# Kernel tuning notes

Hardware: AMD Instinct MI355X
Metric: run time of the kernel (lower is better)

## Reference

```python
import jax, jax.numpy as jnp
import numpy as np

WIDTH = [512, 512, 512, 512]
GRID_SIZE = 5
K = 3  # spline order
GRID_RANGE = (-1.0, 1.0)
BATCH = 1024


def extend_grid(grid, k):
    # grid: (I, G+1) -> (I, G+2k+1), extend k knots on each side with uniform step h
    h = (grid[:, -1:] - grid[:, :1]) / (grid.shape[1] - 1)
    for _ in range(k):
        grid = jnp.concatenate([grid[:, :1] - h, grid, grid[:, -1:] + h], axis=1)
    return grid


def b_spline_basis(x, grid, k):
    # Cox-de Boor recursion. x: (B, I), grid: (I, G+2k+1) -> (B, I, G+k)
    xe = x[:, :, None]
    g = grid[None, :, :]
    B = ((xe >= g[:, :, :-1]) & (xe < g[:, :, 1:])).astype(x.dtype)
    for p in range(1, k + 1):
        B = ((xe - g[:, :, :-(p + 1)]) / (g[:, :, p:-1] - g[:, :, :-(p + 1)]) * B[:, :, :-1]
             + (g[:, :, p + 1:] - xe) / (g[:, :, p + 1:] - g[:, :, 1:-p]) * B[:, :, 1:])
    return B


def kan_layer(x, grid, coef, sb, sp):
    # x: (B, I); coef: (I, O, G+k); sb, sp: (I, O)
    base = jax.nn.silu(x)                              # residual b(x), (B, I)
    Bmat = b_spline_basis(x, grid, K)                  # (B, I, G+k)
    y = jnp.einsum('bik,iok->bio', Bmat, coef)         # spline curves, (B, I, O)
    post = sb[None] * base[:, :, None] + sp[None] * y  # postacts (B, I, O)
    return post.sum(axis=1)                            # (B, O)


def setup_inputs() -> dict:
    key = jax.random.key(0)
    ks = jax.random.split(key, 1 + 2 * (len(WIDTH) - 1))
    inp = {"x": jax.random.normal(ks[0], (BATCH, WIDTH[0]), dtype=jnp.float32)}
    for l, (i, o) in enumerate(zip(WIDTH[:-1], WIDTH[1:])):
        base = jnp.linspace(GRID_RANGE[0], GRID_RANGE[1], GRID_SIZE + 1, dtype=jnp.float32)
        grid = extend_grid(jnp.broadcast_to(base[None], (i, GRID_SIZE + 1)), K)
        kc, kb = ks[1 + 2 * l], ks[2 + 2 * l]
        inp[f"grid{l}"] = grid
        inp[f"coef{l}"] = jax.random.normal(kc, (i, o, GRID_SIZE + K), dtype=jnp.float32) * (0.1 / GRID_SIZE)
        inp[f"sb{l}"] = (jax.random.uniform(kb, (i, o), dtype=jnp.float32) * 2.0 - 1.0) / np.sqrt(i).astype(np.float32)
        inp[f"sp{l}"] = jnp.ones((i, o), dtype=jnp.float32) / np.sqrt(i).astype(np.float32)
    return inp


def reference(x, grid0, coef0, sb0, sp0, grid1, coef1, sb1, sp1, grid2, coef2, sb2, sp2):
    x = kan_layer(x, grid0, coef0, sb0, sp0)
    x = kan_layer(x, grid1, coef1, sb1, sp1)
    x = kan_layer(x, grid2, coef2, sb2, sp2)
    return x
```

## Files before the change

### kernel.cpp

```cpp
#include <hip/hip_runtime.h>
#include <hip/hip_bf16.h>

#define I_DIM  512
#define O_DIM  512
#define NBATCH 1024
#define NSPL   8
#define KPI    12
#define KDIM   (I_DIM * KPI)
#define NGRID  12

typedef __attribute__((ext_vector_type(8))) short bf16x8;
typedef __attribute__((ext_vector_type(4))) float f32x4;

__device__ __forceinline__ void gload_lds16(const __hip_bfloat16* g, __hip_bfloat16* l) {
    __builtin_amdgcn_global_load_lds(
        (const __attribute__((address_space(1))) void*)g,
        (__attribute__((address_space(3))) void*)l, 16, 0, 0);
}

__global__ void build_wt_all(const float* __restrict__ c0, const float* __restrict__ b0, const float* __restrict__ p0,
                             const float* __restrict__ c1, const float* __restrict__ b1, const float* __restrict__ p1,
                             const float* __restrict__ c2, const float* __restrict__ b2, const float* __restrict__ p2,
                             __hip_bfloat16* __restrict__ Wt) {
    int l = blockIdx.y;
    const float* coef = l == 0 ? c0 : (l == 1 ? c1 : c2);
    const float* sb   = l == 0 ? b0 : (l == 1 ? b1 : b2);
    const float* sp   = l == 0 ? p0 : (l == 1 ? p1 : p2);
    __hip_bfloat16* W = Wt + (size_t)l * O_DIM * KDIM;

    int tid = blockIdx.x * blockDim.x + threadIdx.x;
    int i = tid & (I_DIM - 1);
    int o = tid >> 9;
    float sbv = sb[i * O_DIM + o];
    float spv = sp[i * O_DIM + o];
    const float* cf = coef + (size_t)(i * O_DIM + o) * NSPL;
    __align__(16) __hip_bfloat16 row[KPI];
#pragma unroll
    for (int k = 0; k < NSPL; ++k) row[k] = __float2bfloat16(spv * cf[k]);
    __hip_bfloat16 whi = __float2bfloat16(sbv);
    __hip_bfloat16 wlo = __float2bfloat16(sbv - __bfloat162float(whi));
    row[8]  = whi;
    row[9]  = wlo;
    row[10] = whi;
    row[11] = __float2bfloat16(0.0f);
    uint2* dst = (uint2*)(W + (size_t)o * KDIM + i * KPI);
    const uint2* src = (const uint2*)row;
    dst[0] = src[0]; dst[1] = src[1]; dst[2] = src[2];
}

#define SPLITK 8

__device__ __forceinline__ void features_core(float xv, const float* __restrict__ grid,
                                              int i, __hip_bfloat16* __restrict__ dst) {
    float g[NGRID];
#pragma unroll
    for (int j = 0; j < NGRID; ++j) g[j] = grid[i * NGRID + j];

    float B[NGRID - 1];
#pragma unroll
    for (int j = 0; j < NGRID - 1; ++j)
        B[j] = (xv >= g[j] && xv < g[j + 1]) ? 1.0f : 0.0f;
#pragma unroll
    for (int p = 1; p <= 3; ++p) {
#pragma unroll
        for (int j = 0; j < NGRID - 1 - p; ++j) {
            B[j] = (xv - g[j]) / (g[j + p] - g[j]) * B[j]
                 + (g[j + p + 1] - xv) / (g[j + p + 1] - g[j + 1]) * B[j + 1];
        }
    }
    float s = xv / (1.0f + __expf(-xv));
    __hip_bfloat16 shi = __float2bfloat16(s);
    __hip_bfloat16 slo = __float2bfloat16(s - __bfloat162float(shi));

    __align__(16) __hip_bfloat16 row[KPI];
#pragma unroll
    for (int k = 0; k < NSPL; ++k) row[k] = __float2bfloat16(B[k]);
    row[8]  = shi;
    row[9]  = shi;
    row[10] = slo;
    row[11] = __float2bfloat16(0.0f);

    uint2* d = (uint2*)dst;
    const uint2* srow = (const uint2*)row;
    d[0] = srow[0]; d[1] = srow[1]; d[2] = srow[2];
}

__global__ void build_features_x(const float* __restrict__ x,
                                 const float* __restrict__ grid,
                                 __hip_bfloat16* __restrict__ F) {
    int tid = blockIdx.x * blockDim.x + threadIdx.x;
    features_core(x[tid], grid, tid & (I_DIM - 1), F + (size_t)tid * KPI);
}

__global__ void build_features_sum(const float* __restrict__ P,
                                   const float* __restrict__ grid,
                                   __hip_bfloat16* __restrict__ F) {
    int tid = blockIdx.x * blockDim.x + threadIdx.x;
    float xv = 0.f;
#pragma unroll
    for (int s = 0; s < SPLITK; ++s) xv += P[(size_t)s * NBATCH * I_DIM + tid];
    features_core(xv, grid, tid & (I_DIM - 1), F + (size_t)tid * KPI);
}

__global__ void reduce_out(const float* __restrict__ P, float* __restrict__ out) {
    int tid = blockIdx.x * blockDim.x + threadIdx.x;
    float v = 0.f;
#pragma unroll
    for (int s = 0; s < SPLITK; ++s) v += P[(size_t)s * NBATCH * O_DIM + tid];
    out[tid] = v;
}

#define BM 128
#define BN 64
#define BK 64
#define KSEG (KDIM / SPLITK)

__global__ __launch_bounds__(256)
void gemm_kernel(const __hip_bfloat16* __restrict__ A,
                 const __hip_bfloat16* __restrict__ Wt,
                 float* __restrict__ P) {
    __shared__ __hip_bfloat16 lA[BM * BK];
    __shared__ __hip_bfloat16 lB[BN * BK];

    int bm = blockIdx.x;
    int bn = blockIdx.y;
    int ks = blockIdx.z;
    int tid = threadIdx.x;
    int lane = tid & 63;
    int wave = tid >> 6;
    int wr = (wave & 1) * 64;
    int wc = (wave >> 1) * 32;
    int q  = lane >> 4;
    int ln = lane & 15;

    f32x4 acc[4][2];
#pragma unroll
    for (int a = 0; a < 4; ++a)
#pragma unroll
        for (int b = 0; b < 2; ++b) acc[a][b] = (f32x4){0.f, 0.f, 0.f, 0.f};

    const __hip_bfloat16* Abase = A  + (size_t)(bm * BM) * KDIM + ks * KSEG;
    const __hip_bfloat16* Bbase = Wt + (size_t)(bn * BN) * KDIM + ks * KSEG;

    for (int kt = 0; kt < KSEG; kt += BK) {
        __syncthreads();
#pragma unroll
        for (int c = 0; c < 4; ++c) {
            int cc = wave * 256 + c * 64 + lane;
            int r = cc >> 3, j = (cc & 7) ^ (r & 7);
            gload_lds16(Abase + (size_t)r * KDIM + kt + j * 8,
                        lA + (size_t)(wave * 256 + c * 64) * 8);
        }
#pragma unroll
        for (int c = 0; c < 2; ++c) {
            int cc = wave * 128 + c * 64 + lane;
            int r = cc >> 3, j = (cc & 7) ^ (r & 7);
            gload_lds16(Bbase + (size_t)r * KDIM + kt + j * 8,
                        lB + (size_t)(wave * 128 + c * 64) * 8);
        }
        __syncthreads();

#pragma unroll
        for (int kh = 0; kh < 2; ++kh) {
            bf16x8 af[4], bfr[2];
#pragma unroll
            for (int rt = 0; rt < 4; ++rt) {
                int row = wr + rt * 16 + ln;
                af[rt] = *(const bf16x8*)(lA + row * BK + (((kh * 4 + q) ^ (row & 7)) * 8));
            }
#pragma unroll
            for (int ct = 0; ct < 2; ++ct) {
                int row = wc + ct * 16 + ln;
                bfr[ct] = *(const bf16x8*)(lB + row * BK + (((kh * 4 + q) ^ (row & 7)) * 8));
            }
#pragma unroll
            for (int rt = 0; rt < 4; ++rt)
#pragma unroll
                for (int ct = 0; ct < 2; ++ct)
                    acc[rt][ct] = __builtin_amdgcn_mfma_f32_16x16x32_bf16(
                        af[rt], bfr[ct], acc[rt][ct], 0, 0, 0);
        }
    }

    float* Pp = P + (size_t)ks * NBATCH * O_DIM;
    int orow = bm * BM + wr;
    int ocol = bn * BN + wc + ln;
#pragma unroll
    for (int rt = 0; rt < 4; ++rt)
#pragma unroll
        for (int ct = 0; ct < 2; ++ct)
#pragma unroll
            for (int r = 0; r < 4; ++r)
                Pp[(size_t)(orow + rt * 16 + q * 4 + r) * O_DIM + ocol + ct * 16]
                    = acc[rt][ct][r];
}

extern "C" void kernel_launch(void* const* d_in, const int* in_sizes, int n_in,
                              void* d_out, int out_size, void* d_ws, size_t ws_size,
                              hipStream_t stream) {
    const float* x0      = (const float*)d_in[0];
    const float* grid[3] = {(const float*)d_in[1], (const float*)d_in[5], (const float*)d_in[9]};
    const float* coef[3] = {(const float*)d_in[2], (const float*)d_in[6], (const float*)d_in[10]};
    const float* sb[3]   = {(const float*)d_in[3], (const float*)d_in[7], (const float*)d_in[11]};
    const float* sp[3]   = {(const float*)d_in[4], (const float*)d_in[8], (const float*)d_in[12]};

    char* ws = (char*)d_ws;
    const size_t wt_bytes = (size_t)O_DIM * KDIM * sizeof(__hip_bfloat16);
    const size_t f_bytes  = (size_t)NBATCH * KDIM * sizeof(__hip_bfloat16);
    __hip_bfloat16* Wt = (__hip_bfloat16*)ws;
    __hip_bfloat16* F  = (__hip_bfloat16*)(ws + 3 * wt_bytes);
    float* P = (float*)(ws + 3 * wt_bytes + f_bytes);

    build_wt_all<<<dim3((I_DIM * O_DIM) / 256, 3), 256, 0, stream>>>(
        coef[0], sb[0], sp[0], coef[1], sb[1], sp[1], coef[2], sb[2], sp[2], Wt);

    build_features_x<<<(NBATCH * I_DIM) / 256, 256, 0, stream>>>(x0, grid[0], F);
    gemm_kernel<<<dim3(NBATCH / BM, O_DIM / BN, SPLITK), 256, 0, stream>>>(F, Wt, P);

    for (int l = 1; l < 3; ++l) {
        build_features_sum<<<(NBATCH * I_DIM) / 256, 256, 0, stream>>>(P, grid[l], F);
        gemm_kernel<<<dim3(NBATCH / BM, O_DIM / BN, SPLITK), 256, 0, stream>>>(
            F, Wt + (size_t)l * O_DIM * KDIM, P);
    }
    reduce_out<<<(NBATCH * O_DIM) / 256, 256, 0, stream>>>(P, (float*)d_out);
}
```

Before: 202.3 us.

## Fuse all KAN layers into one cooperative persistent kernel with grid syncs

Replaces the sequence of eight separate launches (weight build, feature build, three split-K GEMMs, reductions) with a single cooperative kernel. It uses 256 blocks of 512 threads, and grid-wide barriers separate the phases. The GEMM tile is widened to 128x128 per block so the fixed grid covers every tile, and a fallback launch path is kept if the cooperative launch fails. This removes per-launch overhead and inter-kernel gaps. In exchange, each GEMM phase has fewer, larger blocks with one-block-per-CU occupancy, and grid syncs add their own cost.

Result: slower. 420.0 us (+107.6%).

```diff
diff --git a/kernel.cpp b/kernel.cpp
--- a/kernel.cpp
+++ b/kernel.cpp
@@ -1,5 +1,8 @@
 #include <hip/hip_runtime.h>
 #include <hip/hip_bf16.h>
+#include <hip/hip_cooperative_groups.h>
+
+namespace cg = cooperative_groups;
 
 #define I_DIM  512
 #define O_DIM  512
@@ -8,6 +11,13 @@
 #define KPI    12
 #define KDIM   (I_DIM * KPI)
 #define NGRID  12
+#define SPLITK 8
+#define KSEG   (KDIM / SPLITK)
+#define BK     64
+
+#define NBLK 256
+#define TPB  512
+#define NTH  (NBLK * TPB)
 
 typedef __attribute__((ext_vector_type(8))) short bf16x8;
 typedef __attribute__((ext_vector_type(4))) float f32x4;
@@ -18,19 +28,46 @@
         (__attribute__((address_space(3))) void*)l, 16, 0, 0);
 }
 
-__global__ void build_wt_all(const float* __restrict__ c0, const float* __restrict__ b0, const float* __restrict__ p0,
-                             const float* __restrict__ c1, const float* __restrict__ b1, const float* __restrict__ p1,
-                             const float* __restrict__ c2, const float* __restrict__ b2, const float* __restrict__ p2,
-                             __hip_bfloat16* __restrict__ Wt) {
-    int l = blockIdx.y;
-    const float* coef = l == 0 ? c0 : (l == 1 ? c1 : c2);
-    const float* sb   = l == 0 ? b0 : (l == 1 ? b1 : b2);
-    const float* sp   = l == 0 ? p0 : (l == 1 ? p1 : p2);
-    __hip_bfloat16* W = Wt + (size_t)l * O_DIM * KDIM;
-
-    int tid = blockIdx.x * blockDim.x + threadIdx.x;
-    int i = tid & (I_DIM - 1);
-    int o = tid >> 9;
+__device__ __forceinline__ void features_core(float xv, const float* __restrict__ grid,
+                                              int i, __hip_bfloat16* __restrict__ dst) {
+    float g[NGRID];
+#pragma unroll
+    for (int j = 0; j < NGRID; ++j) g[j] = grid[i * NGRID + j];
+
+    float B[NGRID - 1];
+#pragma unroll
+    for (int j = 0; j < NGRID - 1; ++j)
+        B[j] = (xv >= g[j] && xv < g[j + 1]) ? 1.0f : 0.0f;
+#pragma unroll
+    for (int p = 1; p <= 3; ++p) {
+#pragma unroll
+        for (int j = 0; j < NGRID - 1 - p; ++j) {
+            B[j] = (xv - g[j]) / (g[j + p] - g[j]) * B[j]
+                 + (g[j + p + 1] - xv) / (g[j + p + 1] - g[j + 1]) * B[j + 1];
+        }
+    }
+    float s = xv / (1.0f + __expf(-xv));
+    __hip_bfloat16 shi = __float2bfloat16(s);
+    __hip_bfloat16 slo = __float2bfloat16(s - __bfloat162float(shi));
+
+    __align__(16) __hip_bfloat16 row[KPI];
+#pragma unroll
+    for (int k = 0; k < NSPL; ++k) row[k] = __float2bfloat16(B[k]);
+    row[8]  = shi;
+    row[9]  = shi;
+    row[10] = slo;
+    row[11] = __float2bfloat16(0.0f);
+
+    uint2* d = (uint2*)dst;
+    const uint2* srow = (const uint2*)row;
+    d[0] = srow[0]; d[1] = srow[1]; d[2] = srow[2];
+}
+
+__device__ __forceinline__ void wt_row_core(const float* __restrict__ coef,
+                                            const float* __restrict__ sb,
+                                            const float* __restrict__ sp,
+                                            int i, int o,
+                                            __hip_bfloat16* __restrict__ W) {
     float sbv = sb[i * O_DIM + o];
     float spv = sp[i * O_DIM + o];
     const float* cf = coef + (size_t)(i * O_DIM + o) * NSPL;
@@ -48,41 +85,171 @@
     dst[0] = src[0]; dst[1] = src[1]; dst[2] = src[2];
 }
 
-#define SPLITK 8
-
-__device__ __forceinline__ void features_core(float xv, const float* __restrict__ grid,
-                                              int i, __hip_bfloat16* __restrict__ dst) {
-    float g[NGRID];
-#pragma unroll
-    for (int j = 0; j < NGRID; ++j) g[j] = grid[i * NGRID + j];
-
-    float B[NGRID - 1];
-#pragma unroll
-    for (int j = 0; j < NGRID - 1; ++j)
-        B[j] = (xv >= g[j] && xv < g[j + 1]) ? 1.0f : 0.0f;
-#pragma unroll
-    for (int p = 1; p <= 3; ++p) {
-#pragma unroll
-        for (int j = 0; j < NGRID - 1 - p; ++j) {
-            B[j] = (xv - g[j]) / (g[j + p] - g[j]) * B[j]
-                 + (g[j + p + 1] - xv) / (g[j + p + 1] - g[j + 1]) * B[j + 1];
-        }
-    }
-    float s = xv / (1.0f + __expf(-xv));
-    __hip_bfloat16 shi = __float2bfloat16(s);
-    __hip_bfloat16 slo = __float2bfloat16(s - __bfloat162float(shi));
-
-    __align__(16) __hip_bfloat16 row[KPI];
-#pragma unroll
-    for (int k = 0; k < NSPL; ++k) row[k] = __float2bfloat16(B[k]);
-    row[8]  = shi;
-    row[9]  = shi;
-    row[10] = slo;
-    row[11] = __float2bfloat16(0.0f);
-
-    uint2* d = (uint2*)dst;
-    const uint2* srow = (const uint2*)row;
-    d[0] = srow[0]; d[1] = srow[1]; d[2] = srow[2];
+__device__ __forceinline__ void gemm_tile8(const __hip_bfloat16* __restrict__ A,
+                                           const __hip_bfloat16* __restrict__ W,
+                                           float* __restrict__ P,
+                                           __hip_bfloat16* lA, __hip_bfloat16* lB,
+                                           int bid, int tid) {
+    int bm = bid >> 5;
+    int bn = (bid >> 3) & 3;
+    int ks = bid & 7;
+    int lane = tid & 63;
+    int wave = tid >> 6;
+    int wr = (wave & 1) * 64;
+    int wc = (wave >> 1) * 32;
+    int q  = lane >> 4;
+    int ln = lane & 15;
+
+    f32x4 acc[4][2];
+#pragma unroll
+    for (int a = 0; a < 4; ++a)
+#pragma unroll
+        for (int b = 0; b < 2; ++b) acc[a][b] = (f32x4){0.f, 0.f, 0.f, 0.f};
+
+    const __hip_bfloat16* Abase = A + (size_t)(bm * 128) * KDIM + ks * KSEG;
+    const __hip_bfloat16* Bbase = W + (size_t)(bn * 128) * KDIM + ks * KSEG;
+
+    for (int kt = 0; kt < KSEG; kt += BK) {
+        __syncthreads();
+#pragma unroll
+        for (int c = 0; c < 2; ++c) {
+            int cc = wave * 128 + c * 64 + lane;
+            int r = cc >> 3, j = (cc & 7) ^ (r & 7);
+            gload_lds16(Abase + (size_t)r * KDIM + kt + j * 8,
+                        lA + (size_t)(wave * 128 + c * 64) * 8);
+        }
+#pragma unroll
+        for (int c = 0; c < 2; ++c) {
+            int cc = wave * 128 + c * 64 + lane;
+            int r = cc >> 3, j = (cc & 7) ^ (r & 7);
+            gload_lds16(Bbase + (size_t)r * KDIM + kt + j * 8,
+                        lB + (size_t)(wave * 128 + c * 64) * 8);
+        }
+        __syncthreads();
+
+#pragma unroll
+        for (int kh = 0; kh < 2; ++kh) {
+            bf16x8 af[4], bfr[2];
+#pragma unroll
+            for (int rt = 0; rt < 4; ++rt) {
+                int row = wr + rt * 16 + ln;
+                af[rt] = *(const bf16x8*)(lA + row * BK + (((kh * 4 + q) ^ (row & 7)) * 8));
+            }
+#pragma unroll
+            for (int ct = 0; ct < 2; ++ct) {
+                int row = wc + ct * 16 + ln;
+                bfr[ct] = *(const bf16x8*)(lB + row * BK + (((kh * 4 + q) ^ (row & 7)) * 8));
+            }
+#pragma unroll
+            for (int rt = 0; rt < 4; ++rt)
+#pragma unroll
+                for (int ct = 0; ct < 2; ++ct)
+                    acc[rt][ct] = __builtin_amdgcn_mfma_f32_16x16x32_bf16(
+                        af[rt], bfr[ct], acc[rt][ct], 0, 0, 0);
+        }
+    }
+
+    float* Pp = P + (size_t)ks * NBATCH * O_DIM;
+    int orow = bm * 128 + wr;
+    int ocol = bn * 128 + wc + ln;
+#pragma unroll
+    for (int rt = 0; rt < 4; ++rt)
+#pragma unroll
+        for (int ct = 0; ct < 2; ++ct)
+#pragma unroll
+            for (int r = 0; r < 4; ++r)
+                Pp[(size_t)(orow + rt * 16 + q * 4 + r) * O_DIM + ocol + ct * 16]
+                    = acc[rt][ct][r];
+}
+
+__global__ __launch_bounds__(TPB, 2)
+void kan_fused(const float* __restrict__ x0,
+               const float* __restrict__ gr0, const float* __restrict__ gr1,
+               const float* __restrict__ gr2,
+               const float* __restrict__ c0, const float* __restrict__ sb0, const float* __restrict__ sp0,
+               const float* __restrict__ c1, const float* __restrict__ sb1, const float* __restrict__ sp1,
+               const float* __restrict__ c2, const float* __restrict__ sb2, const float* __restrict__ sp2,
+               __hip_bfloat16* __restrict__ Wt,
+               __hip_bfloat16* __restrict__ F,
+               float* __restrict__ P,
+               float* __restrict__ out) {
+    __shared__ __hip_bfloat16 lA[128 * BK];
+    __shared__ __hip_bfloat16 lB[128 * BK];
+
+    cg::grid_group gg = cg::this_grid();
+    const int tid  = threadIdx.x;
+    const int bid  = blockIdx.x;
+    const int gtid = bid * TPB + tid;
+
+#pragma unroll
+    for (int it = 0; it < 6; ++it) {
+        int e = gtid + it * NTH;
+        int l = e >> 18;
+        const float* coef = l == 0 ? c0  : (l == 1 ? c1  : c2);
+        const float* sb   = l == 0 ? sb0 : (l == 1 ? sb1 : sb2);
+        const float* sp   = l == 0 ? sp0 : (l == 1 ? sp1 : sp2);
+        int rem = e & (I_DIM * O_DIM - 1);
+        wt_row_core(coef, sb, sp, rem & (I_DIM - 1), rem >> 9,
+                    Wt + (size_t)l * O_DIM * KDIM);
+    }
+
+#pragma unroll
+    for (int it = 0; it < 4; ++it) {
+        int e = gtid + it * NTH;
+        features_core(x0[e], gr0, e & (I_DIM - 1), F + (size_t)e * KPI);
+    }
+    gg.sync();
+
+    gemm_tile8(F, Wt, P, lA, lB, bid, tid);
+    gg.sync();
+
+#pragma unroll
+    for (int it = 0; it < 4; ++it) {
+        int e = gtid + it * NTH;
+        float xv = 0.f;
+#pragma unroll
+        for (int s = 0; s < SPLITK; ++s) xv += P[(size_t)s * NBATCH * I_DIM + e];
+        features_core(xv, gr1, e & (I_DIM - 1), F + (size_t)e * KPI);
+    }
+    gg.sync();
+
+    gemm_tile8(F, Wt + (size_t)O_DIM * KDIM, P, lA, lB, bid, tid);
+    gg.sync();
+
+#pragma unroll
+    for (int it = 0; it < 4; ++it) {
+        int e = gtid + it * NTH;
+        float xv = 0.f;
+#pragma unroll
+        for (int s = 0; s < SPLITK; ++s) xv += P[(size_t)s * NBATCH * I_DIM + e];
+        features_core(xv, gr2, e & (I_DIM - 1), F + (size_t)e * KPI);
+    }
+    gg.sync();
+
+    gemm_tile8(F, Wt + (size_t)2 * O_DIM * KDIM, P, lA, lB, bid, tid);
+    gg.sync();
+
+#pragma unroll
+    for (int it = 0; it < 4; ++it) {
+        int e = gtid + it * NTH;
+        float v = 0.f;
+#pragma unroll
+        for (int s = 0; s < SPLITK; ++s) v += P[(size_t)s * NBATCH * O_DIM + e];
+        out[e] = v;
+    }
+}
+
+__global__ void build_wt_all(const float* __restrict__ c0, const float* __restrict__ b0, const float* __restrict__ p0,
+                             const float* __restrict__ c1, const float* __restrict__ b1, const float* __restrict__ p1,
+                             const float* __restrict__ c2, const float* __restrict__ b2, const float* __restrict__ p2,
+                             __hip_bfloat16* __restrict__ Wt) {
+    int l = blockIdx.y;
+    const float* coef = l == 0 ? c0 : (l == 1 ? c1 : c2);
+    const float* sb   = l == 0 ? b0 : (l == 1 ? b1 : b2);
+    const float* sp   = l == 0 ? p0 : (l == 1 ? p1 : p2);
+    int tid = blockIdx.x * blockDim.x + threadIdx.x;
+    wt_row_core(coef, sb, sp, tid & (I_DIM - 1), tid >> 9,
+                Wt + (size_t)l * O_DIM * KDIM);
 }
 
 __global__ void build_features_x(const float* __restrict__ x,
@@ -110,17 +277,12 @@
     out[tid] = v;
 }
 
-#define BM 128
-#define BN 64
-#define BK 64
-#define KSEG (KDIM / SPLITK)
-
 __global__ __launch_bounds__(256)
-void gemm_kernel(const __hip_bfloat16* __restrict__ A,
-                 const __hip_bfloat16* __restrict__ Wt,
-                 float* __restrict__ P) {
-    __shared__ __hip_bfloat16 lA[BM * BK];
-    __shared__ __hip_bfloat16 lB[BN * BK];
+void gemm_kernel_fb(const __hip_bfloat16* __restrict__ A,
+                    const __hip_bfloat16* __restrict__ Wt,
+                    float* __restrict__ P) {
+    __shared__ __hip_bfloat16 lA[128 * BK];
+    __shared__ __hip_bfloat16 lB[64 * BK];
 
     int bm = blockIdx.x;
     int bn = blockIdx.y;
@@ -139,8 +301,8 @@
 #pragma unroll
         for (int b = 0; b < 2; ++b) acc[a][b] = (f32x4){0.f, 0.f, 0.f, 0.f};
 
-    const __hip_bfloat16* Abase = A  + (size_t)(bm * BM) * KDIM + ks * KSEG;
-    const __hip_bfloat16* Bbase = Wt + (size_t)(bn * BN) * KDIM + ks * KSEG;
+    const __hip_bfloat16* Abase = A  + (size_t)(bm * 128) * KDIM + ks * KSEG;
+    const __hip_bfloat16* Bbase = Wt + (size_t)(bn * 64) * KDIM + ks * KSEG;
 
     for (int kt = 0; kt < KSEG; kt += BK) {
         __syncthreads();
@@ -183,8 +345,8 @@
     }
 
     float* Pp = P + (size_t)ks * NBATCH * O_DIM;
-    int orow = bm * BM + wr;
-    int ocol = bn * BN + wc + ln;
+    int orow = bm * 128 + wr;
+    int ocol = bn * 64 + wc + ln;
 #pragma unroll
     for (int rt = 0; rt < 4; ++rt)
 #pragma unroll
@@ -198,11 +360,19 @@
 extern "C" void kernel_launch(void* const* d_in, const int* in_sizes, int n_in,
                               void* d_out, int out_size, void* d_ws, size_t ws_size,
                               hipStream_t stream) {
-    const float* x0      = (const float*)d_in[0];
-    const float* grid[3] = {(const float*)d_in[1], (const float*)d_in[5], (const float*)d_in[9]};
-    const float* coef[3] = {(const float*)d_in[2], (const float*)d_in[6], (const float*)d_in[10]};
-    const float* sb[3]   = {(const float*)d_in[3], (const float*)d_in[7], (const float*)d_in[11]};
-    const float* sp[3]   = {(const float*)d_in[4], (const float*)d_in[8], (const float*)d_in[12]};
+    const float* x0  = (const float*)d_in[0];
+    const float* gr0 = (const float*)d_in[1];
+    const float* c0  = (const float*)d_in[2];
+    const float* sb0 = (const float*)d_in[3];
+    const float* sp0 = (const float*)d_in[4];
+    const float* gr1 = (const float*)d_in[5];
+    const float* c1  = (const float*)d_in[6];
+    const float* sb1 = (const float*)d_in[7];
+    const float* sp1 = (const float*)d_in[8];
+    const float* gr2 = (const float*)d_in[9];
+    const float* c2  = (const float*)d_in[10];
+    const float* sb2 = (const float*)d_in[11];
+    const float* sp2 = (const float*)d_in[12];
 
     char* ws = (char*)d_ws;
     const size_t wt_bytes = (size_t)O_DIM * KDIM * sizeof(__hip_bfloat16);
@@ -210,17 +380,26 @@
     __hip_bfloat16* Wt = (__hip_bfloat16*)ws;
     __hip_bfloat16* F  = (__hip_bfloat16*)(ws + 3 * wt_bytes);
     float* P = (float*)(ws + 3 * wt_bytes + f_bytes);
-
-    build_wt_all<<<dim3((I_DIM * O_DIM) / 256, 3), 256, 0, stream>>>(
-        coef[0], sb[0], sp[0], coef[1], sb[1], sp[1], coef[2], sb[2], sp[2], Wt);
-
-    build_features_x<<<(NBATCH * I_DIM) / 256, 256, 0, stream>>>(x0, grid[0], F);
-    gemm_kernel<<<dim3(NBATCH / BM, O_DIM / BN, SPLITK), 256, 0, stream>>>(F, Wt, P);
-
-    for (int l = 1; l < 3; ++l) {
-        build_features_sum<<<(NBATCH * I_DIM) / 256, 256, 0, stream>>>(P, grid[l], F);
-        gemm_kernel<<<dim3(NBATCH / BM, O_DIM / BN, SPLITK), 256, 0, stream>>>(
-            F, Wt + (size_t)l * O_DIM * KDIM, P);
-    }
-    reduce_out<<<(NBATCH * O_DIM) / 256, 256, 0, stream>>>(P, (float*)d_out);
-}
+    float* out = (float*)d_out;
+
+    void* args[] = {&x0, &gr0, &gr1, &gr2,
+                    &c0, &sb0, &sp0, &c1, &sb1, &sp1, &c2, &sb2, &sp2,
+                    &Wt, &F, &P, &out};
+
+    hipError_t err = hipLaunchCooperativeKernel(
+        reinterpret_cast<const void*>(kan_fused),
+        dim3(NBLK), dim3(TPB), args, 0, stream);
+
+    if (err != hipSuccess) {
+        (void)hipGetLastError();
+        build_wt_all<<<dim3((I_DIM * O_DIM) / 256, 3), 256, 0, stream>>>(
+            c0, sb0, sp0, c1, sb1, sp1, c2, sb2, sp2, Wt);
+        build_features_x<<<(NBATCH * I_DIM) / 256, 256, 0, stream>>>(x0, gr0, F);
+        gemm_kernel_fb<<<dim3(8, 8, SPLITK), 256, 0, stream>>>(F, Wt, P);
+        build_features_sum<<<(NBATCH * I_DIM) / 256, 256, 0, stream>>>(P, gr1, F);
+        gemm_kernel_fb<<<dim3(8, 8, SPLITK), 256, 0, stream>>>(F, Wt + (size_t)O_DIM * KDIM, P);
+        build_features_sum<<<(NBATCH * I_DIM) / 256, 256, 0, stream>>>(P, gr2, F);
+        gemm_kernel_fb<<<dim3(8, 8, SPLITK), 256, 0, stream>>>(F, Wt + (size_t)2 * O_DIM * KDIM, P);
+        reduce_out<<<(NBATCH * O_DIM) / 256, 256, 0, stream>>>(P, out);
+    }
+}
```

## Fuse weight and first-layer feature prep, shrink GEMM tile and halve split-K

Applied to the files above, without the earlier changes.

The weight-building kernel and the first-layer feature kernel are merged into one prep launch. The weight build now maps a block to 64 inputs by 4 outputs, which changes how sb, sp and coef are read. The GEMM tile drops from 128x64 to 64x64 and split-K goes from 8 to 4, keeping the block count the same while halving the partial-sum traffic read by the feature and reduce kernels. In exchange, each GEMM block runs twice as many k-iterations with less reuse per LDS tile, and the new weight mapping makes the transposed stores to Wt scattered.

After: 199.9 us. Within noise of the previous version (-1.2%).

```diff
diff --git a/kernel.cpp b/kernel.cpp
--- a/kernel.cpp
+++ b/kernel.cpp
@@ -9,6 +9,12 @@
 #define KDIM   (I_DIM * KPI)
 #define NGRID  12
 
+#define SPLITK 4
+#define KSEG   (KDIM / SPLITK)
+#define BK     64
+#define BM     64
+#define BN     64
+
 typedef __attribute__((ext_vector_type(8))) short bf16x8;
 typedef __attribute__((ext_vector_type(4))) float f32x4;
 
@@ -18,19 +24,46 @@
         (__attribute__((address_space(3))) void*)l, 16, 0, 0);
 }
 
-__global__ void build_wt_all(const float* __restrict__ c0, const float* __restrict__ b0, const float* __restrict__ p0,
-                             const float* __restrict__ c1, const float* __restrict__ b1, const float* __restrict__ p1,
-                             const float* __restrict__ c2, const float* __restrict__ b2, const float* __restrict__ p2,
-                             __hip_bfloat16* __restrict__ Wt) {
-    int l = blockIdx.y;
-    const float* coef = l == 0 ? c0 : (l == 1 ? c1 : c2);
-    const float* sb   = l == 0 ? b0 : (l == 1 ? b1 : b2);
-    const float* sp   = l == 0 ? p0 : (l == 1 ? p1 : p2);
-    __hip_bfloat16* W = Wt + (size_t)l * O_DIM * KDIM;
-
-    int tid = blockIdx.x * blockDim.x + threadIdx.x;
-    int i = tid & (I_DIM - 1);
-    int o = tid >> 9;
+__device__ __forceinline__ void features_core(float xv, const float* __restrict__ grid,
+                                              int i, __hip_bfloat16* __restrict__ dst) {
+    float g[NGRID];
+#pragma unroll
+    for (int j = 0; j < NGRID; ++j) g[j] = grid[i * NGRID + j];
+
+    float B[NGRID - 1];
+#pragma unroll
+    for (int j = 0; j < NGRID - 1; ++j)
+        B[j] = (xv >= g[j] && xv < g[j + 1]) ? 1.0f : 0.0f;
+#pragma unroll
+    for (int p = 1; p <= 3; ++p) {
+#pragma unroll
+        for (int j = 0; j < NGRID - 1 - p; ++j) {
+            B[j] = (xv - g[j]) / (g[j + p] - g[j]) * B[j]
+                 + (g[j + p + 1] - xv) / (g[j + p + 1] - g[j + 1]) * B[j + 1];
+        }
+    }
+    float s = xv / (1.0f + __expf(-xv));
+    __hip_bfloat16 shi = __float2bfloat16(s);
+    __hip_bfloat16 slo = __float2bfloat16(s - __bfloat162float(shi));
+
+    __align__(16) __hip_bfloat16 row[KPI];
+#pragma unroll
+    for (int k = 0; k < NSPL; ++k) row[k] = __float2bfloat16(B[k]);
+    row[8]  = shi;
+    row[9]  = shi;
+    row[10] = slo;
+    row[11] = __float2bfloat16(0.0f);
+
+    uint2* d = (uint2*)dst;
+    const uint2* srow = (const uint2*)row;
+    d[0] = srow[0]; d[1] = srow[1]; d[2] = srow[2];
+}
+
+__device__ __forceinline__ void wt_row_core(const float* __restrict__ coef,
+                                            const float* __restrict__ sb,
+                                            const float* __restrict__ sp,
+                                            int i, int o,
+                                            __hip_bfloat16* __restrict__ W) {
     float sbv = sb[i * O_DIM + o];
     float spv = sp[i * O_DIM + o];
     const float* cf = coef + (size_t)(i * O_DIM + o) * NSPL;
@@ -48,53 +81,37 @@
     dst[0] = src[0]; dst[1] = src[1]; dst[2] = src[2];
 }
 
-#define SPLITK 8
-
-__device__ __forceinline__ void features_core(float xv, const float* __restrict__ grid,
-                                              int i, __hip_bfloat16* __restrict__ dst) {
-    float g[NGRID];
-#pragma unroll
-    for (int j = 0; j < NGRID; ++j) g[j] = grid[i * NGRID + j];
-
-    float B[NGRID - 1];
-#pragma unroll
-    for (int j = 0; j < NGRID - 1; ++j)
-        B[j] = (xv >= g[j] && xv < g[j + 1]) ? 1.0f : 0.0f;
-#pragma unroll
-    for (int p = 1; p <= 3; ++p) {
-#pragma unroll
-        for (int j = 0; j < NGRID - 1 - p; ++j) {
-            B[j] = (xv - g[j]) / (g[j + p] - g[j]) * B[j]
-                 + (g[j + p + 1] - xv) / (g[j + p + 1] - g[j + 1]) * B[j + 1];
-        }
+#define WT_BLOCKS   3072
+#define FEAT_BLOCKS 2048
+__global__ __launch_bounds__(256)
+void prep_kernel(const float* __restrict__ x0, const float* __restrict__ gr0,
+                 const float* __restrict__ c0, const float* __restrict__ sb0, const float* __restrict__ sp0,
+                 const float* __restrict__ c1, const float* __restrict__ sb1, const float* __restrict__ sp1,
+                 const float* __restrict__ c2, const float* __restrict__ sb2, const float* __restrict__ sp2,
+                 __hip_bfloat16* __restrict__ Wt,
+                 __hip_bfloat16* __restrict__ F) {
+    int b = blockIdx.x;
+    int t = threadIdx.x;
+    if (b < WT_BLOCKS) {
+        int l   = b >> 10;
+        int rem = b & 1023;
+        int i0  = (rem & 7) * 64;
+        int o0  = (rem >> 3) * 4;
+        const float* coef = l == 0 ? c0  : (l == 1 ? c1  : c2);
+        const float* sb   = l == 0 ? sb0 : (l == 1 ? sb1 : sb2);
+        const float* sp   = l == 0 ? sp0 : (l == 1 ? sp1 : sp2);
+        wt_row_core(coef, sb, sp, i0 + (t >> 2), o0 + (t & 3),
+                    Wt + (size_t)l * O_DIM * KDIM);
+    } else {
+        int e = (b - WT_BLOCKS) * 256 + t;
+        features_core(x0[e], gr0, e & (I_DIM - 1), F + (size_t)e * KPI);
     }
-    float s = xv / (1.0f + __expf(-xv));
-    __hip_bfloat16 shi = __float2bfloat16(s);
-    __hip_bfloat16 slo = __float2bfloat16(s - __bfloat162float(shi));
-
-    __align__(16) __hip_bfloat16 row[KPI];
-#pragma unroll
-    for (int k = 0; k < NSPL; ++k) row[k] = __float2bfloat16(B[k]);
-    row[8]  = shi;
-    row[9]  = shi;
-    row[10] = slo;
-    row[11] = __float2bfloat16(0.0f);
-
-    uint2* d = (uint2*)dst;
-    const uint2* srow = (const uint2*)row;
-    d[0] = srow[0]; d[1] = srow[1]; d[2] = srow[2];
-}
-
-__global__ void build_features_x(const float* __restrict__ x,
-                                 const float* __restrict__ grid,
-                                 __hip_bfloat16* __restrict__ F) {
-    int tid = blockIdx.x * blockDim.x + threadIdx.x;
-    features_core(x[tid], grid, tid & (I_DIM - 1), F + (size_t)tid * KPI);
-}
-
-__global__ void build_features_sum(const float* __restrict__ P,
-                                   const float* __restrict__ grid,
-                                   __hip_bfloat16* __restrict__ F) {
+}
+
+__global__ __launch_bounds__(256)
+void build_features_sum(const float* __restrict__ P,
+                        const float* __restrict__ grid,
+                        __hip_bfloat16* __restrict__ F) {
     int tid = blockIdx.x * blockDim.x + threadIdx.x;
     float xv = 0.f;
 #pragma unroll
@@ -102,18 +119,14 @@
     features_core(xv, grid, tid & (I_DIM - 1), F + (size_t)tid * KPI);
 }
 
-__global__ void reduce_out(const float* __restrict__ P, float* __restrict__ out) {
+__global__ __launch_bounds__(256)
+void reduce_out(const float* __restrict__ P, float* __restrict__ out) {
     int tid = blockIdx.x * blockDim.x + threadIdx.x;
     float v = 0.f;
 #pragma unroll
     for (int s = 0; s < SPLITK; ++s) v += P[(size_t)s * NBATCH * O_DIM + tid];
     out[tid] = v;
 }
-
-#define BM 128
-#define BN 64
-#define BK 64
-#define KSEG (KDIM / SPLITK)
 
 __global__ __launch_bounds__(256)
 void gemm_kernel(const __hip_bfloat16* __restrict__ A,
@@ -128,14 +141,14 @@
     int tid = threadIdx.x;
     int lane = tid & 63;
     int wave = tid >> 6;
-    int wr = (wave & 1) * 64;
+    int wr = (wave & 1) * 32;
     int wc = (wave >> 1) * 32;
     int q  = lane >> 4;
     int ln = lane & 15;
 
-    f32x4 acc[4][2];
-#pragma unroll
-    for (int a = 0; a < 4; ++a)
+    f32x4 acc[2][2];
+#pragma unroll
+    for (int a = 0; a < 2; ++a)
 #pragma unroll
         for (int b = 0; b < 2; ++b) acc[a][b] = (f32x4){0.f, 0.f, 0.f, 0.f};
 
@@ -145,11 +158,11 @@
     for (int kt = 0; kt < KSEG; kt += BK) {
         __syncthreads();
 #pragma unroll
-        for (int c = 0; c < 4; ++c) {
-            int cc = wave * 256 + c * 64 + lane;
+        for (int c = 0; c < 2; ++c) {
+            int cc = wave * 128 + c * 64 + lane;
             int r = cc >> 3, j = (cc & 7) ^ (r & 7);
             gload_lds16(Abase + (size_t)r * KDIM + kt + j * 8,
-                        lA + (size_t)(wave * 256 + c * 64) * 8);
+                        lA + (size_t)(wave * 128 + c * 64) * 8);
         }
 #pragma unroll
         for (int c = 0; c < 2; ++c) {
@@ -162,9 +175,9 @@
 
 #pragma unroll
         for (int kh = 0; kh < 2; ++kh) {
-            bf16x8 af[4], bfr[2];
-#pragma unroll
-            for (int rt = 0; rt < 4; ++rt) {
+            bf16x8 af[2], bfr[2];
+#pragma unroll
+            for (int rt = 0; rt < 2; ++rt) {
                 int row = wr + rt * 16 + ln;
                 af[rt] = *(const bf16x8*)(lA + row * BK + (((kh * 4 + q) ^ (row & 7)) * 8));
             }
@@ -174,7 +187,7 @@
                 bfr[ct] = *(const bf16x8*)(lB + row * BK + (((kh * 4 + q) ^ (row & 7)) * 8));
             }
 #pragma unroll
-            for (int rt = 0; rt < 4; ++rt)
+            for (int rt = 0; rt < 2; ++rt)
 #pragma unroll
                 for (int ct = 0; ct < 2; ++ct)
                     acc[rt][ct] = __builtin_amdgcn_mfma_f32_16x16x32_bf16(
@@ -186,7 +199,7 @@
     int orow = bm * BM + wr;
     int ocol = bn * BN + wc + ln;
 #pragma unroll
-    for (int rt = 0; rt < 4; ++rt)
+    for (int rt = 0; rt < 2; ++rt)
 #pragma unroll
         for (int ct = 0; ct < 2; ++ct)
 #pragma unroll
@@ -198,11 +211,19 @@
 extern "C" void kernel_launch(void* const* d_in, const int* in_sizes, int n_in,
                               void* d_out, int out_size, void* d_ws, size_t ws_size,
                               hipStream_t stream) {
-    const float* x0      = (const float*)d_in[0];
-    const float* grid[3] = {(const float*)d_in[1], (const float*)d_in[5], (const float*)d_in[9]};
-    const float* coef[3] = {(const float*)d_in[2], (const float*)d_in[6], (const float*)d_in[10]};
-    const float* sb[3]   = {(const float*)d_in[3], (const float*)d_in[7], (const float*)d_in[11]};
-    const float* sp[3]   = {(const float*)d_in[4], (const float*)d_in[8], (const float*)d_in[12]};
+    const float* x0  = (const float*)d_in[0];
+    const float* gr0 = (const float*)d_in[1];
+    const float* c0  = (const float*)d_in[2];
+    const float* sb0 = (const float*)d_in[3];
+    const float* sp0 = (const float*)d_in[4];
+    const float* gr1 = (const float*)d_in[5];
+    const float* c1  = (const float*)d_in[6];
+    const float* sb1 = (const float*)d_in[7];
+    const float* sp1 = (const float*)d_in[8];
+    const float* gr2 = (const float*)d_in[9];
+    const float* c2  = (const float*)d_in[10];
+    const float* sb2 = (const float*)d_in[11];
+    const float* sp2 = (const float*)d_in[12];
 
     char* ws = (char*)d_ws;
     const size_t wt_bytes = (size_t)O_DIM * KDIM * sizeof(__hip_bfloat16);
@@ -210,17 +231,20 @@
     __hip_bfloat16* Wt = (__hip_bfloat16*)ws;
     __hip_bfloat16* F  = (__hip_bfloat16*)(ws + 3 * wt_bytes);
     float* P = (float*)(ws + 3 * wt_bytes + f_bytes);
-
-    build_wt_all<<<dim3((I_DIM * O_DIM) / 256, 3), 256, 0, stream>>>(
-        coef[0], sb[0], sp[0], coef[1], sb[1], sp[1], coef[2], sb[2], sp[2], Wt);
-
-    build_features_x<<<(NBATCH * I_DIM) / 256, 256, 0, stream>>>(x0, grid[0], F);
+    float* out = (float*)d_out;
+
+    prep_kernel<<<WT_BLOCKS + FEAT_BLOCKS, 256, 0, stream>>>(
+        x0, gr0, c0, sb0, sp0, c1, sb1, sp1, c2, sb2, sp2, Wt, F);
+
     gemm_kernel<<<dim3(NBATCH / BM, O_DIM / BN, SPLITK), 256, 0, stream>>>(F, Wt, P);
 
-    for (int l = 1; l < 3; ++l) {
-        build_features_sum<<<(NBATCH * I_DIM) / 256, 256, 0, stream>>>(P, grid[l], F);
-        gemm_kernel<<<dim3(NBATCH / BM, O_DIM / BN, SPLITK), 256, 0, stream>>>(
-            F, Wt + (size_t)l * O_DIM * KDIM, P);
-    }
-    reduce_out<<<(NBATCH * O_DIM) / 256, 256, 0, stream>>>(P, (float*)d_out);
-}
+    build_features_sum<<<(NBATCH * I_DIM) / 256, 256, 0, stream>>>(P, gr1, F);
+    gemm_kernel<<<dim3(NBATCH / BM, O_DIM / BN, SPLITK), 256, 0, stream>>>(
+        F, Wt + (size_t)O_DIM * KDIM, P);
+
+    build_features_sum<<<(NBATCH * I_DIM) / 256, 256, 0, stream>>>(P, gr2, F);
+    gemm_kernel<<<dim3(NBATCH / BM, O_DIM / BN, SPLITK), 256, 0, stream>>>(
+        F, Wt + (size_t)2 * O_DIM * KDIM, P);
+
+    reduce_out<<<(NBATCH * O_DIM) / 256, 256, 0, stream>>>(P, out);
+}
```
